# Optimization experiments

Hardware: AMD Instinct MI355X
Metric: run time of the kernel (lower is better)

Reference implementation:

```python
import jax, jax.numpy as jnp
import numpy as np

ENC, STR_H, CELL_H, ATTN = 512, 256, 512, 512
B, L = 64, 1024


def setup_inputs() -> dict:
    key = jax.random.key(0)
    ks = jax.random.split(key, 12)
    s = lambda fan_in: 1.0 / np.sqrt(fan_in)
    return {
        "encoded_features_map": jax.random.normal(ks[0], (B, L, ENC), jnp.float32),
        "structural_hidden_state": jax.random.normal(ks[1], (1, B, STR_H), jnp.float32),
        "cell_content_hidden_state": jax.random.normal(ks[2], (1, B, CELL_H), jnp.float32),
        "W_enc": jax.random.uniform(ks[3], (ENC, ATTN), jnp.float32, -s(ENC), s(ENC)),
        "b_enc": jax.random.uniform(ks[4], (ATTN,), jnp.float32, -s(ENC), s(ENC)),
        "W_str": jax.random.uniform(ks[5], (STR_H, ATTN), jnp.float32, -s(STR_H), s(STR_H)),
        "b_str": jax.random.uniform(ks[6], (ATTN,), jnp.float32, -s(STR_H), s(STR_H)),
        "W_cell": jax.random.uniform(ks[7], (CELL_H, ATTN), jnp.float32, -s(CELL_H), s(CELL_H)),
        "b_cell": jax.random.uniform(ks[8], (ATTN,), jnp.float32, -s(CELL_H), s(CELL_H)),
        "W_comb": jax.random.uniform(ks[9], (ATTN, 1), jnp.float32, -s(ATTN), s(ATTN)),
        "b_comb": jax.random.uniform(ks[10], (1,), jnp.float32, -s(ATTN), s(ATTN)),
    }


def reference(encoded_features_map, structural_hidden_state, cell_content_hidden_state,
              W_enc, b_enc, W_str, b_str, W_cell, b_cell, W_comb, b_comb):
    # [B, L, A] projection of encoder features
    a_enc = jnp.einsum("ble,ea->bla", encoded_features_map, W_enc) + b_enc
    # [B, A] projections of the two hidden states (squeeze layer dim)
    a_str = structural_hidden_state[0] @ W_str + b_str
    a_cell = cell_content_hidden_state[0] @ W_cell + b_cell
    # broadcast add + ReLU + scalar score: [B, L]
    h = jax.nn.relu(a_enc + a_str[:, None, :] + a_cell[:, None, :])
    scores = jnp.einsum("bla,ao->bl", h, W_comb) + b_comb[0]
    weights = jax.nn.softmax(scores, axis=1)  # over sequence dim
    # weighted sum over L -> [B, ENC]
    context = jnp.einsum("bl,ble->be", weights, encoded_features_map)
    return context
```

## Files before the change

### kernel.cpp

```cpp
#include <hip/hip_runtime.h>
#include <stdint.h>

#define ENC_D 512
#define ATTN_D 512
#define STR_D 256
#define CELL_D 512
#define BATCH 64
#define SEQ 1024
#define NROWS (BATCH * SEQ)

typedef __bf16 bf16x8 __attribute__((ext_vector_type(8)));
typedef float f32x4 __attribute__((ext_vector_type(4)));

__device__ __forceinline__ unsigned short f2bf(float f) {
    unsigned int u = __float_as_uint(f);
    u += 0x7fffu + ((u >> 16) & 1u);
    return (unsigned short)(u >> 16);
}

__device__ __forceinline__ void lds_cp16(void* l, const void* g) {
    __builtin_amdgcn_global_load_lds(
        (const __attribute__((address_space(1))) unsigned int*)g,
        (__attribute__((address_space(3))) unsigned int*)l, 16, 0, 0);
}

__global__ __launch_bounds__(256) void k_prep(const float* __restrict__ W,
                                              unsigned short* __restrict__ WF,
                                              const float* __restrict__ str,
                                              const float* __restrict__ cell,
                                              const float* __restrict__ Wstr,
                                              const float* __restrict__ Wcell,
                                              float* __restrict__ bpart,
                                              float* __restrict__ outz) {
    __shared__ char smraw[64 * 68 * 2];
    const int bx = blockIdx.x, t = threadIdx.x;

    if (bx < 64) {
        unsigned short* T = (unsigned short*)smraw;
        const int ei = bx >> 3, ni = bx & 7;
        const int e0 = ei * 64, n0 = ni * 64;
#pragma unroll
        for (int i = 0; i < 4; ++i) {
            const int idx = t + i * 256;
            const int r = idx >> 4, c4 = idx & 15;
            const float4 v = *(const float4*)(W + (size_t)(e0 + r) * ATTN_D + n0 + c4 * 4);
            T[(c4 * 4 + 0) * 68 + r] = f2bf(v.x);
            T[(c4 * 4 + 1) * 68 + r] = f2bf(v.y);
            T[(c4 * 4 + 2) * 68 + r] = f2bf(v.z);
            T[(c4 * 4 + 3) * 68 + r] = f2bf(v.w);
        }
        __syncthreads();
#pragma unroll
        for (int i = 0; i < 2; ++i) {
            const int q = t + i * 256;
            const int n = q >> 3, ge = q & 7;
            union { unsigned short s[8]; uint4 u; } o;
#pragma unroll
            for (int j = 0; j < 8; ++j) o.s[j] = T[n * 68 + ge * 8 + j];
            const int ng = n0 + n;
            const int g = ei * 8 + ge;
            const int nt = ng >> 4, c = ng & 15;
            const int ks = g >> 2, quad = g & 3;
            const int gi = nt * 1024 + ks * 64 + quad * 16 + c;
            *(uint4*)(WF + (size_t)gi * 8) = o.u;
        }
    } else if (bx < 832) {
        float* sj = (float*)smraw;
        float* red = (float*)smraw + 64;
        const int q = bx - 64;
        const int b = q / 12, jq = q - b * 12;
        const float* hvec;
        const float* Wbase;
        if (jq < 4) { hvec = str + b * STR_D + jq * 64;         Wbase = Wstr + (size_t)(jq * 64) * ATTN_D; }
        else        { hvec = cell + b * CELL_D + (jq - 4) * 64; Wbase = Wcell + (size_t)((jq - 4) * 64) * ATTN_D; }
        if (t < 64) sj[t] = hvec[t];
        __syncthreads();
        const int h = t >> 7, a4 = t & 127;
        f32x4 acc = {0.f, 0.f, 0.f, 0.f};
#pragma unroll 8
        for (int i = h * 32; i < h * 32 + 32; ++i) {
            const float s = sj[i];
            const float4 wv = *(const float4*)(Wbase + (size_t)i * ATTN_D + a4 * 4);
            acc[0] += s * wv.x; acc[1] += s * wv.y; acc[2] += s * wv.z; acc[3] += s * wv.w;
        }
        if (h == 1) *(f32x4*)(red + a4 * 4) = acc;
        __syncthreads();
        if (h == 0) {
            const f32x4 o = *(const f32x4*)(red + a4 * 4);
            acc[0] += o[0]; acc[1] += o[1]; acc[2] += o[2]; acc[3] += o[3];
            *(f32x4*)(bpart + (size_t)(jq * BATCH + b) * ATTN_D + a4 * 4) = acc;
        }
    } else {
        const f32x4 z = {0.f, 0.f, 0.f, 0.f};
        float* p = outz + (size_t)(bx - 832) * 2048 + t * 8;
        *(f32x4*)p = z;
        *(f32x4*)(p + 4) = z;
    }
}

__global__ __launch_bounds__(512, 2) void k_scores(const float* __restrict__ E,
                                                   const unsigned short* __restrict__ WF,
                                                   const float* __restrict__ bpart,
                                                   const float* __restrict__ b_enc,
                                                   const float* __restrict__ b_str,
                                                   const float* __restrict__ b_cell,
                                                   const float* __restrict__ Wcomb,
                                                   float* __restrict__ scores) {
    __shared__ unsigned short buf[2][8192];
    __shared__ float sbias[512];
    __shared__ float sWc[512];

    const int tid = threadIdx.x;
    const int r0 = blockIdx.x * 256;
    const int b = blockIdx.x >> 2;
    const int w = tid >> 6, lane = tid & 63;
    const int quad = lane >> 4, c = lane & 15;

#pragma unroll
    for (int i = 0; i < 2; ++i)
        lds_cp16((char*)&buf[0][0] + i * 8192 + tid * 16,
                 (const char*)WF + i * 8192 + tid * 16);

    if (tid < 128) {
        const int a = tid * 4;
        const float4 be = *(const float4*)(b_enc + a);
        const float4 bs = *(const float4*)(b_str + a);
        const float4 bc = *(const float4*)(b_cell + a);
        f32x4 s;
        s[0] = be.x + bs.x + bc.x; s[1] = be.y + bs.y + bc.y;
        s[2] = be.z + bs.z + bc.z; s[3] = be.w + bs.w + bc.w;
#pragma unroll
        for (int jq = 0; jq < 12; ++jq) {
            const float4 p = *(const float4*)(bpart + (size_t)(jq * BATCH + b) * ATTN_D + a);
            s[0] += p.x; s[1] += p.y; s[2] += p.z; s[3] += p.w;
        }
        *(f32x4*)(sbias + a) = s;
        const float4 wcv = *(const float4*)(Wcomb + a);
        f32x4 wc4; wc4[0] = wcv.x; wc4[1] = wcv.y; wc4[2] = wcv.z; wc4[3] = wcv.w;
        *(f32x4*)(sWc + a) = wc4;
    }

    bf16x8 afr[2][16];
#pragma unroll
    for (int m = 0; m < 2; ++m) {
        const float* Ep = E + (size_t)(r0 + w * 32 + m * 16 + c) * ENC_D + quad * 8;
#pragma unroll
        for (int ks = 0; ks < 16; ++ks) {
            const float4 v0 = *(const float4*)(Ep + ks * 32);
            const float4 v1 = *(const float4*)(Ep + ks * 32 + 4);
            union { unsigned short s[8]; bf16x8 v; } u;
            u.s[0] = f2bf(v0.x); u.s[1] = f2bf(v0.y);
            u.s[2] = f2bf(v0.z); u.s[3] = f2bf(v0.w);
            u.s[4] = f2bf(v1.x); u.s[5] = f2bf(v1.y);
            u.s[6] = f2bf(v1.z); u.s[7] = f2bf(v1.w);
            afr[m][ks] = u.v;
        }
    }

    float sc0[4] = {0.f, 0.f, 0.f, 0.f};
    float sc1[4] = {0.f, 0.f, 0.f, 0.f};

    __syncthreads();

    for (int ch = 0; ch < 32; ++ch) {
        if (ch < 31) {
            const char* gsrc = (const char*)WF + (size_t)(ch + 1) * 16384;
            char* ldst = (char*)&buf[(ch + 1) & 1][0];
#pragma unroll
            for (int i = 0; i < 2; ++i)
                lds_cp16(ldst + i * 8192 + tid * 16, gsrc + i * 8192 + tid * 16);
        }

        const unsigned short* wb = &buf[ch & 1][0];
        f32x4 a0 = {0.f, 0.f, 0.f, 0.f}, a1 = {0.f, 0.f, 0.f, 0.f};
#pragma unroll
        for (int ks = 0; ks < 16; ++ks) {
            const bf16x8 b0 = *(const bf16x8*)(wb + (ks * 64 + lane) * 8);
            a0 = __builtin_amdgcn_mfma_f32_16x16x32_bf16(afr[0][ks], b0, a0, 0, 0, 0);
            a1 = __builtin_amdgcn_mfma_f32_16x16x32_bf16(afr[1][ks], b0, a1, 0, 0, 0);
        }

        const int n = ch * 16 + c;
        const float bi = sbias[n], wc = sWc[n];
#pragma unroll
        for (int r = 0; r < 4; ++r) {
            float v;
            v = a0[r] + bi; sc0[r] += (v > 0.f ? v : 0.f) * wc;
            v = a1[r] + bi; sc1[r] += (v > 0.f ? v : 0.f) * wc;
        }
        __syncthreads();
    }

#pragma unroll
    for (int r = 0; r < 4; ++r) {
        float v0 = sc0[r], v1 = sc1[r];
        v0 += __shfl_xor(v0, 1); v1 += __shfl_xor(v1, 1);
        v0 += __shfl_xor(v0, 2); v1 += __shfl_xor(v1, 2);
        v0 += __shfl_xor(v0, 4); v1 += __shfl_xor(v1, 4);
        sc0[r] = v0 + __shfl_xor(v0, 8);
        sc1[r] = v1 + __shfl_xor(v1, 8);
    }
    if (c == 0) {
        const int g0 = r0 + w * 32 + quad * 4;
#pragma unroll
        for (int r = 0; r < 4; ++r) scores[g0 + r] = sc0[r];
#pragma unroll
        for (int r = 0; r < 4; ++r) scores[g0 + 16 + r] = sc1[r];
    }
}

__global__ __launch_bounds__(128) void k_ctx(const float* __restrict__ E,
                                             const float* __restrict__ scores,
                                             float* __restrict__ out) {
    __shared__ float ex[1024];
    __shared__ float rtmp[4];
    const int blk = blockIdx.x, t = threadIdx.x;
    const int b = blk >> 4, lo = blk & 15;

    float v[8];
    float m = -1e30f;
#pragma unroll
    for (int i = 0; i < 8; ++i) {
        v[i] = scores[b * SEQ + i * 128 + t];
        m = fmaxf(m, v[i]);
    }
#pragma unroll
    for (int o = 32; o > 0; o >>= 1) m = fmaxf(m, __shfl_xor(m, o));
    if ((t & 63) == 0) rtmp[t >> 6] = m;
    __syncthreads();
    m = fmaxf(rtmp[0], rtmp[1]);

    float s = 0.f;
#pragma unroll
    for (int i = 0; i < 8; ++i) {
        const float e = __expf(v[i] - m);
        ex[i * 128 + t] = e;
        s += e;
    }
#pragma unroll
    for (int o = 32; o > 0; o >>= 1) s += __shfl_xor(s, o);
    if ((t & 63) == 0) rtmp[2 + (t >> 6)] = s;
    __syncthreads();
    const float inv = 1.f / (rtmp[2] + rtmp[3]);

    const float* Ep = E + (size_t)(b * SEQ + lo * 64) * ENC_D + t * 4;
    f32x4 acc = {0.f, 0.f, 0.f, 0.f};
#pragma unroll 8
    for (int l = 0; l < 64; ++l) {
        const float4 e4 = *(const float4*)(Ep + (size_t)l * ENC_D);
        const float wv = ex[lo * 64 + l];
        acc[0] += wv * e4.x; acc[1] += wv * e4.y;
        acc[2] += wv * e4.z; acc[3] += wv * e4.w;
    }
    float* op = out + b * ENC_D + t * 4;
    atomicAdd(op + 0, acc[0] * inv);
    atomicAdd(op + 1, acc[1] * inv);
    atomicAdd(op + 2, acc[2] * inv);
    atomicAdd(op + 3, acc[3] * inv);
}

extern "C" void kernel_launch(void* const* d_in, const int* in_sizes, int n_in,
                              void* d_out, int out_size, void* d_ws, size_t ws_size,
                              hipStream_t stream) {
    const float* E      = (const float*)d_in[0];
    const float* str    = (const float*)d_in[1];
    const float* cell   = (const float*)d_in[2];
    const float* Wenc   = (const float*)d_in[3];
    const float* b_enc  = (const float*)d_in[4];
    const float* Wstr   = (const float*)d_in[5];
    const float* b_str  = (const float*)d_in[6];
    const float* Wcell  = (const float*)d_in[7];
    const float* b_cell = (const float*)d_in[8];
    const float* Wcomb  = (const float*)d_in[9];
    float* out = (float*)d_out;

    char* ws = (char*)d_ws;
    unsigned short* WF = (unsigned short*)ws;
    float* scores = (float*)(ws + (512 << 10));
    float* bpart  = (float*)(ws + (512 << 10) + (256 << 10));

    k_prep<<<848, 256, 0, stream>>>(Wenc, WF, str, cell, Wstr, Wcell, bpart, out);
    k_scores<<<NROWS / 256, 512, 0, stream>>>(E, WF, bpart, b_enc, b_str, b_cell, Wcomb, scores);
    k_ctx<<<1024, 128, 0, stream>>>(E, scores, out);
}
```

Before: 281.6 us.

## Triple-buffer 32-column weight chunks with partial vmcnt barriers in score kernel

The score kernel now stages 32 output columns of bf16 weights per chunk instead of 16, using a three-deep LDS ring with prefetch distance two. The plain __syncthreads is replaced by an s_waitcnt vmcnt(4) plus s_barrier, so the newest prefetch can stay in flight across the barrier. Each chunk splits its MFMA chain into even and odd k accumulators for more independent work. Launch bounds drop from 2 to 1 block per CU to make room for the larger LDS footprint and the extra accumulator registers, which reduces occupancy and latency hiding.

```diff
diff --git a/kernel.cpp b/kernel.cpp
--- a/kernel.cpp
+++ b/kernel.cpp
@@ -23,6 +23,9 @@
         (const __attribute__((address_space(1))) unsigned int*)g,
         (__attribute__((address_space(3))) unsigned int*)l, 16, 0, 0);
 }
+
+#define BAR_VM4() asm volatile("s_waitcnt vmcnt(4)\n\ts_barrier" ::: "memory")
+#define BAR_VM0() asm volatile("s_waitcnt vmcnt(0)\n\ts_barrier" ::: "memory")
 
 __global__ __launch_bounds__(256) void k_prep(const float* __restrict__ W,
                                               unsigned short* __restrict__ WF,
@@ -98,7 +101,7 @@
     }
 }
 
-__global__ __launch_bounds__(512, 2) void k_scores(const float* __restrict__ E,
+__global__ __launch_bounds__(512, 1) void k_scores(const float* __restrict__ E,
                                                    const unsigned short* __restrict__ WF,
                                                    const float* __restrict__ bpart,
                                                    const float* __restrict__ b_enc,
@@ -106,7 +109,7 @@
                                                    const float* __restrict__ b_cell,
                                                    const float* __restrict__ Wcomb,
                                                    float* __restrict__ scores) {
-    __shared__ unsigned short buf[2][8192];
+    __shared__ unsigned short buf[3][16384];
     __shared__ float sbias[512];
     __shared__ float sWc[512];
 
@@ -117,9 +120,11 @@
     const int quad = lane >> 4, c = lane & 15;
 
 #pragma unroll
-    for (int i = 0; i < 2; ++i)
-        lds_cp16((char*)&buf[0][0] + i * 8192 + tid * 16,
-                 (const char*)WF + i * 8192 + tid * 16);
+    for (int p = 0; p < 2; ++p)
+#pragma unroll
+        for (int i = 0; i < 4; ++i)
+            lds_cp16((char*)&buf[p][0] + i * 8192 + tid * 16,
+                     (const char*)WF + (size_t)p * 32768 + i * 8192 + tid * 16);
 
     if (tid < 128) {
         const int a = tid * 4;
@@ -162,33 +167,55 @@
 
     __syncthreads();
 
-    for (int ch = 0; ch < 32; ++ch) {
-        if (ch < 31) {
-            const char* gsrc = (const char*)WF + (size_t)(ch + 1) * 16384;
-            char* ldst = (char*)&buf[(ch + 1) & 1][0];
-#pragma unroll
-            for (int i = 0; i < 2; ++i)
+    int cbuf = 0, sbuf = 2;
+    for (int ch = 0; ch < 16; ++ch) {
+        if (ch < 14) {
+            const char* gsrc = (const char*)WF + (size_t)(ch + 2) * 32768;
+            char* ldst = (char*)&buf[sbuf][0];
+#pragma unroll
+            for (int i = 0; i < 4; ++i)
                 lds_cp16(ldst + i * 8192 + tid * 16, gsrc + i * 8192 + tid * 16);
         }
 
-        const unsigned short* wb = &buf[ch & 1][0];
-        f32x4 a0 = {0.f, 0.f, 0.f, 0.f}, a1 = {0.f, 0.f, 0.f, 0.f};
-#pragma unroll
-        for (int ks = 0; ks < 16; ++ks) {
-            const bf16x8 b0 = *(const bf16x8*)(wb + (ks * 64 + lane) * 8);
-            a0 = __builtin_amdgcn_mfma_f32_16x16x32_bf16(afr[0][ks], b0, a0, 0, 0, 0);
-            a1 = __builtin_amdgcn_mfma_f32_16x16x32_bf16(afr[1][ks], b0, a1, 0, 0, 0);
-        }
-
-        const int n = ch * 16 + c;
-        const float bi = sbias[n], wc = sWc[n];
+        const unsigned short* wb = &buf[cbuf][0];
+        f32x4 a0e = {0.f,0.f,0.f,0.f}, a0o = {0.f,0.f,0.f,0.f};
+        f32x4 a1e = {0.f,0.f,0.f,0.f}, a1o = {0.f,0.f,0.f,0.f};
+        f32x4 b0e = {0.f,0.f,0.f,0.f}, b0o = {0.f,0.f,0.f,0.f};
+        f32x4 b1e = {0.f,0.f,0.f,0.f}, b1o = {0.f,0.f,0.f,0.f};
+#pragma unroll
+        for (int ks = 0; ks < 16; ks += 2) {
+            const bf16x8 f0 = *(const bf16x8*)(wb + (ks * 64 + lane) * 8);
+            const bf16x8 f1 = *(const bf16x8*)(wb + ((ks + 1) * 64 + lane) * 8);
+            const bf16x8 g0 = *(const bf16x8*)(wb + 8192 + (ks * 64 + lane) * 8);
+            const bf16x8 g1 = *(const bf16x8*)(wb + 8192 + ((ks + 1) * 64 + lane) * 8);
+            a0e = __builtin_amdgcn_mfma_f32_16x16x32_bf16(afr[0][ks], f0, a0e, 0, 0, 0);
+            a1e = __builtin_amdgcn_mfma_f32_16x16x32_bf16(afr[1][ks], f0, a1e, 0, 0, 0);
+            a0o = __builtin_amdgcn_mfma_f32_16x16x32_bf16(afr[0][ks + 1], f1, a0o, 0, 0, 0);
+            a1o = __builtin_amdgcn_mfma_f32_16x16x32_bf16(afr[1][ks + 1], f1, a1o, 0, 0, 0);
+            b0e = __builtin_amdgcn_mfma_f32_16x16x32_bf16(afr[0][ks], g0, b0e, 0, 0, 0);
+            b1e = __builtin_amdgcn_mfma_f32_16x16x32_bf16(afr[1][ks], g0, b1e, 0, 0, 0);
+            b0o = __builtin_amdgcn_mfma_f32_16x16x32_bf16(afr[0][ks + 1], g1, b0o, 0, 0, 0);
+            b1o = __builtin_amdgcn_mfma_f32_16x16x32_bf16(afr[1][ks + 1], g1, b1o, 0, 0, 0);
+        }
+
+        const int n0 = ch * 32 + c;
+        const float bi0 = sbias[n0], wc0 = sWc[n0];
+        const float bi1 = sbias[n0 + 16], wc1 = sWc[n0 + 16];
 #pragma unroll
         for (int r = 0; r < 4; ++r) {
             float v;
-            v = a0[r] + bi; sc0[r] += (v > 0.f ? v : 0.f) * wc;
-            v = a1[r] + bi; sc1[r] += (v > 0.f ? v : 0.f) * wc;
-        }
-        __syncthreads();
+            v = (a0e[r] + a0o[r]) + bi0; sc0[r] += (v > 0.f ? v : 0.f) * wc0;
+            v = (b0e[r] + b0o[r]) + bi1; sc0[r] += (v > 0.f ? v : 0.f) * wc1;
+            v = (a1e[r] + a1o[r]) + bi0; sc1[r] += (v > 0.f ? v : 0.f) * wc0;
+            v = (b1e[r] + b1o[r]) + bi1; sc1[r] += (v > 0.f ? v : 0.f) * wc1;
+        }
+
+        cbuf = (cbuf == 2) ? 0 : cbuf + 1;
+        sbuf = (sbuf == 2) ? 0 : sbuf + 1;
+        if (ch < 15) {
+            if (ch < 14) BAR_VM4();
+            else         BAR_VM0();
+        }
     }
 
 #pragma unroll
```

Measured after the change: 274.7 us. 2.5% less time.
